# Performance work log

Hardware: AMD Instinct MI355X
Metric: run time of the kernel (lower is better)

The kernel has to match this reference:

```python
import jax, jax.numpy as jnp
import numpy as np

HEAD = 4      # args.head
N_HOPS = 2    # n_hops == gt_layer


def setup_inputs() -> dict:
    key = jax.random.key(0)
    ks = jax.random.split(key, 8)
    N, D, E, R = 100000, 64, 800000, 32
    entity_emb = jax.random.normal(ks[0], (N, D), dtype=jnp.float32) * 0.1
    weight = jax.random.normal(ks[1], (R - 1, D), dtype=jnp.float32) * 0.1
    Wq = jax.random.normal(ks[2], (N_HOPS, D, D), dtype=jnp.float32) * (1.0 / np.sqrt(D))
    Wk = jax.random.normal(ks[3], (N_HOPS, D, D), dtype=jnp.float32) * (1.0 / np.sqrt(D))
    Wv = jax.random.normal(ks[4], (N_HOPS, D, D), dtype=jnp.float32) * (1.0 / np.sqrt(D))
    edge_index = jax.random.randint(ks[5], (2, E), 0, N, dtype=jnp.int64 if jax.config.jax_enable_x64 else jnp.int32)
    edge_type = jax.random.randint(ks[6], (E,), 1, R, dtype=edge_index.dtype)  # in [1, R-1]
    return {"entity_emb": entity_emb, "weight": weight, "Wq": Wq, "Wk": Wk,
            "Wv": Wv, "edge_index": edge_index, "edge_type": edge_type}


def _kg_layer(rows, col_embeds, embeds, n_nodes, wq, wk, wv):
    # per-edge scaled-dot attention with index_add softmax normalization
    E, D = col_embeds.shape
    dh = D // HEAD
    q = (embeds[rows] @ wq).reshape(E, HEAD, dh)
    k = (col_embeds @ wk).reshape(E, HEAD, dh)
    v = (col_embeds @ wv).reshape(E, HEAD, dh)
    att = jnp.clip(jnp.einsum('ehd,ehd->eh', q, k), -10.0, 10.0)
    exp_att = jnp.exp(att)                                        # [E, H]
    att_norm = jax.ops.segment_sum(exp_att, rows, num_segments=n_nodes)[rows]
    a = exp_att / (att_norm + 1e-8)
    res = (a[..., None] * v).reshape(E, D)
    return jax.ops.segment_sum(res, rows, num_segments=n_nodes)   # [N, D]


def _scatter_softmax(x, index, n_seg):
    # numerically-stable softmax over edges grouped by index (torch_scatter.scatter_softmax)
    m = jax.ops.segment_max(x, index, num_segments=n_seg)
    e = jnp.exp(x - m[index])
    s = jax.ops.segment_sum(e, index, num_segments=n_seg)
    return e / (s[index] + 1e-16)


def reference(entity_emb, weight, Wq, Wk, Wv, edge_index, edge_type):
    N, D = entity_emb.shape
    head, tail = edge_index[0], edge_index[1]
    rel = weight[edge_type - 1]                                   # [E, D]
    emb = entity_emb
    res = entity_emb
    for layer in range(N_HOPS):
        neigh_rel = emb[tail] * rel                               # [E, D]
        kg_emb = _kg_layer(head, neigh_rel, emb, N, Wq[layer], Wk[layer], Wv[layer])
        # calculate_sim_hrt: product of L2 norms, squared (scalar per edge)
        hn = jnp.linalg.norm(kg_emb[head] * rel, axis=1)
        tn = jnp.linalg.norm(kg_emb[tail] * rel, axis=1)
        w = (hn * tn) ** 2                                        # [E]
        a = _scatter_softmax(w, head, N)                          # [E]
        neigh = a[:, None] * emb[tail]                            # [E, D]
        agg = jax.ops.segment_sum(neigh, head, num_segments=N)    # [N, D]
        # F.normalize + residual accumulation across hops
        emb = agg / jnp.maximum(jnp.linalg.norm(agg, axis=1, keepdims=True), 1e-12)
        res = res + emb
    return res
```

## Files before the change

### kernel.cpp

```cpp
#include <hip/hip_runtime.h>
#include <hip/hip_fp16.h>
#include <math.h>

#define BD 256
#define PBLK 2048

#define RED16(v) { v += __shfl_xor(v, 1, 64); v += __shfl_xor(v, 2, 64); \
                   v += __shfl_xor(v, 4, 64); v += __shfl_xor(v, 8, 64); }
#define REDQ(v)  { v += __shfl_xor(v, 16, 64); v += __shfl_xor(v, 32, 64); }

__device__ __forceinline__ __half2 shflxor_h2(__half2 v, int off) {
  int i = __shfl_xor(*(int*)&v, off, 64);
  return *(__half2*)&i;
}
#define REDQH(v)  { v = __hadd2(v, shflxor_h2(v, 16)); v = __hadd2(v, shflxor_h2(v, 32)); }
#define RED16H(v) { v = __hadd2(v, shflxor_h2(v, 1)); v = __hadd2(v, shflxor_h2(v, 2)); \
                    v = __hadd2(v, shflxor_h2(v, 4)); v = __hadd2(v, shflxor_h2(v, 8)); }

__global__ void k_init(const float4* __restrict__ ent, uint2* __restrict__ e16,
                       float4* __restrict__ out, int n4, int* __restrict__ deg, int N) {
  int i = blockIdx.x * BD + threadIdx.x;
  if (i < n4) {
    float4 v = ent[i];
    out[i] = v;
    __half2 h01 = __floats2half2_rn(v.x, v.y);
    __half2 h23 = __floats2half2_rn(v.z, v.w);
    uint2 st; st.x = *(unsigned int*)&h01; st.y = *(unsigned int*)&h23;
    e16[i] = st;
  }
  if (i < N) deg[i] = 0;
}

__global__ void k_deg(const int* __restrict__ head, int* __restrict__ deg, int E) {
  int e = blockIdx.x * BD + threadIdx.x;
  if (e < E) atomicAdd(&deg[head[e]], 1);
}

__global__ void k_scan_a(const int* __restrict__ deg, int* __restrict__ rowptr,
                         int* __restrict__ bsum, int N) {
  __shared__ int s[BD];
  int t = threadIdx.x, i = blockIdx.x * BD + t;
  int v = (i < N) ? deg[i] : 0;
  s[t] = v; __syncthreads();
  for (int off = 1; off < BD; off <<= 1) {
    int add = (t >= off) ? s[t - off] : 0;
    __syncthreads();
    s[t] += add;
    __syncthreads();
  }
  if (i < N) rowptr[i] = s[t] - v;
  if (t == BD - 1) bsum[blockIdx.x] = s[t];
}

__global__ void k_scan_b(const int* __restrict__ bsum, int* __restrict__ boff, int nb) {
  __shared__ int s[512];
  int t = threadIdx.x;
  int v = (t < nb) ? bsum[t] : 0;
  s[t] = v; __syncthreads();
  for (int off = 1; off < 512; off <<= 1) {
    int add = (t >= off) ? s[t - off] : 0;
    __syncthreads();
    s[t] += add;
    __syncthreads();
  }
  boff[t] = s[t] - v;
}

__global__ void k_scan_c(int* __restrict__ rowptr, int* __restrict__ cur,
                         const int* __restrict__ boff, int N, int E) {
  int i = blockIdx.x * BD + threadIdx.x;
  if (i < N) { int v = rowptr[i] + boff[blockIdx.x]; rowptr[i] = v; cur[i] = v; }
  if (i == 0) rowptr[N] = E;
}

__global__ void k_scatter(const int* __restrict__ head, const int* __restrict__ tail,
                          const int* __restrict__ etype,
                          int* __restrict__ cur, int2* __restrict__ epack, int E) {
  int e = blockIdx.x * BD + threadIdx.x;
  if (e < E) {
    int p = atomicAdd(&cur[head[e]], 1);
    epack[p] = make_int2(tail[e], etype[e] - 1);
  }
}

__global__ void k_m(const float* __restrict__ Wq, const float* __restrict__ Wk,
                    const float* __restrict__ weight,
                    float* __restrict__ Mf, __half* __restrict__ w16) {
  int tid = blockIdx.x * BD + threadIdx.x;
  int c = tid & 255;
  int m = tid >> 8;
  int i = c >> 2, h = c & 3;
  const float* wq = Wq + m * 64 + h * 16;
  const float* wk = Wk + i * 64 + h * 16;
  float acc = 0.f;
#pragma unroll
  for (int d = 0; d < 16; d++) acc = fmaf(wq[d], wk[d], acc);
  Mf[tid] = acc;
  if (tid < 2048) {
    int r = tid >> 6, j = tid & 63;
    w16[tid] = __float2half((r < 31) ? weight[r * 64 + j] : 0.f);
  }
}

__global__ __launch_bounds__(256) void k_g(const __half* __restrict__ e16,
                                           const float* __restrict__ Mf,
                                           uint2* __restrict__ Gh2, int N) {
  __shared__ float lM[64 * 256];
  int t = threadIdx.x;
  const float4* Mf4 = (const float4*)Mf;
  float4* lM4 = (float4*)lM;
  for (int i = t; i < 4096; i += BD) lM4[i] = Mf4[i];
  __syncthreads();
  int lane = t & 63, w = t >> 6;
  int nloc0 = blockIdx.x * 64 + w * 16;
#pragma unroll
  for (int b = 0; b < 2; b++) {
    int nl = nloc0 + b * 8;
    float4 acc[8];
#pragma unroll
    for (int ni = 0; ni < 8; ni++) acc[ni] = make_float4(0.f, 0.f, 0.f, 0.f);
#pragma unroll 4
    for (int m = 0; m < 64; m += 2) {
      float4 Mv0 = lM4[m * 64 + lane];
      float4 Mv1 = lM4[(m + 1) * 64 + lane];
#pragma unroll
      for (int ni = 0; ni < 8; ni++) {
        __half2 eh = *(const __half2*)(e16 + (size_t)(nl + ni) * 64 + m);
        float2 ef = __half22float2(eh);
        acc[ni].x = fmaf(ef.x, Mv0.x, acc[ni].x);
        acc[ni].y = fmaf(ef.x, Mv0.y, acc[ni].y);
        acc[ni].z = fmaf(ef.x, Mv0.z, acc[ni].z);
        acc[ni].w = fmaf(ef.x, Mv0.w, acc[ni].w);
        acc[ni].x = fmaf(ef.y, Mv1.x, acc[ni].x);
        acc[ni].y = fmaf(ef.y, Mv1.y, acc[ni].y);
        acc[ni].z = fmaf(ef.y, Mv1.z, acc[ni].z);
        acc[ni].w = fmaf(ef.y, Mv1.w, acc[ni].w);
      }
    }
#pragma unroll
    for (int ni = 0; ni < 8; ni++)
      if (nl + ni < N) {
        __half2 h01 = __floats2half2_rn(acc[ni].x, acc[ni].y);
        __half2 h23 = __floats2half2_rn(acc[ni].z, acc[ni].w);
        uint2 st;
        st.x = *(unsigned int*)&h01;
        st.y = *(unsigned int*)&h23;
        Gh2[(size_t)(nl + ni) * 64 + lane] = st;
      }
  }
}

__global__ __launch_bounds__(256) void k_fused(const uint2* __restrict__ e16,
                        const uint2* __restrict__ w16,
                        const uint4* __restrict__ Ghq, const float* __restrict__ Wv,
                        const int2* __restrict__ epack, const int* __restrict__ rowptr,
                        float* __restrict__ kg, int N) {
  __shared__ float SL[4 * 272];
  int t = threadIdx.x, lane = t & 63, w = t >> 6, q = lane >> 4, s = lane & 15;
  float* L = SL + w * 272;
  int wid = blockIdx.x * 4 + w, nw = gridDim.x * 4;
  const __half2 z2 = __float2half2_rn(0.f);
  for (int n = wid; n < N; n += nw) {
    uint4 ga = Ghq[(size_t)n * 32 + s * 2];
    uint4 gb = Ghq[(size_t)n * 32 + s * 2 + 1];
    __half2 c0h01 = *(__half2*)&ga.x, c0h23 = *(__half2*)&ga.y;
    __half2 c1h01 = *(__half2*)&ga.z, c1h23 = *(__half2*)&ga.w;
    __half2 c2h01 = *(__half2*)&gb.x, c2h23 = *(__half2*)&gb.y;
    __half2 c3h01 = *(__half2*)&gb.z, c3h23 = *(__half2*)&gb.w;

    int base = rowptr[n], deg = rowptr[n + 1] - base;
    float4 den = make_float4(0.f, 0.f, 0.f, 0.f);
    __half2 S0a = z2, S0b = z2, S1a = z2, S1b = z2;
    __half2 S2a = z2, S2b = z2, S3a = z2, S3b = z2;
    for (int g0 = 0; g0 < deg; g0 += 4) {
      int k = g0 + q;
      bool valid = (k < deg);
      int kk = min(k, deg - 1);
      int2 p = epack[base + kk];
      uint2 eu = e16[(size_t)p.x * 16 + s];
      uint2 ru = w16[(size_t)p.y * 16 + s];
      __half2 x01 = __hmul2(*(__half2*)&eu.x, *(__half2*)&ru.x);
      __half2 x23 = __hmul2(*(__half2*)&eu.y, *(__half2*)&ru.y);
      __half2 b0 = __low2half2(x01), b1 = __high2half2(x01);
      __half2 b2 = __low2half2(x23), b3 = __high2half2(x23);
      __half2 a01 = __hmul2(b0, c0h01);
      a01 = __hfma2(b1, c1h01, a01);
      a01 = __hfma2(b2, c2h01, a01);
      a01 = __hfma2(b3, c3h01, a01);
      __half2 a23 = __hmul2(b0, c0h23);
      a23 = __hfma2(b1, c1h23, a23);
      a23 = __hfma2(b2, c2h23, a23);
      a23 = __hfma2(b3, c3h23, a23);
      RED16H(a01) RED16H(a23)
      float2 fa01 = __half22float2(a01);
      float2 fa23 = __half22float2(a23);
      fa01.x = fminf(10.f, fmaxf(-10.f, fa01.x));
      fa01.y = fminf(10.f, fmaxf(-10.f, fa01.y));
      fa23.x = fminf(10.f, fmaxf(-10.f, fa23.x));
      fa23.y = fminf(10.f, fmaxf(-10.f, fa23.y));
      float4 ev;
      ev.x = valid ? __expf(fa01.x) : 0.f;
      ev.y = valid ? __expf(fa01.y) : 0.f;
      ev.z = valid ? __expf(fa23.x) : 0.f;
      ev.w = valid ? __expf(fa23.y) : 0.f;
      den.x += ev.x; den.y += ev.y; den.z += ev.z; den.w += ev.w;
      __half2 e01 = __floats2half2_rn(ev.x, ev.y);
      __half2 e23 = __floats2half2_rn(ev.z, ev.w);
      S0a = __hfma2(e01, b0, S0a); S0b = __hfma2(e23, b0, S0b);
      S1a = __hfma2(e01, b1, S1a); S1b = __hfma2(e23, b1, S1b);
      S2a = __hfma2(e01, b2, S2a); S2b = __hfma2(e23, b2, S2b);
      S3a = __hfma2(e01, b3, S3a); S3b = __hfma2(e23, b3, S3b);
    }
    REDQ(den.x) REDQ(den.y) REDQ(den.z) REDQ(den.w)
    REDQH(S0a) REDQH(S0b) REDQH(S1a) REDQH(S1b)
    REDQH(S2a) REDQH(S2b) REDQH(S3a) REDQH(S3b)
    float4 inv;
    inv.x = 1.f / (den.x + 1e-8f); inv.y = 1.f / (den.y + 1e-8f);
    inv.z = 1.f / (den.z + 1e-8f); inv.w = 1.f / (den.w + 1e-8f);
    float2 c0, c1;
    c0 = __half22float2(S0a); c1 = __half22float2(S0b);
    float s0h0 = c0.x * inv.x, s0h1 = c0.y * inv.y, s0h2 = c1.x * inv.z, s0h3 = c1.y * inv.w;
    c0 = __half22float2(S1a); c1 = __half22float2(S1b);
    float s1h0 = c0.x * inv.x, s1h1 = c0.y * inv.y, s1h2 = c1.x * inv.z, s1h3 = c1.y * inv.w;
    c0 = __half22float2(S2a); c1 = __half22float2(S2b);
    float s2h0 = c0.x * inv.x, s2h1 = c0.y * inv.y, s2h2 = c1.x * inv.z, s2h3 = c1.y * inv.w;
    c0 = __half22float2(S3a); c1 = __half22float2(S3b);
    float s3h0 = c0.x * inv.x, s3h1 = c0.y * inv.y, s3h2 = c1.x * inv.z, s3h3 = c1.y * inv.w;
    if (q == 0) {
      *(float4*)(L +       s * 4) = make_float4(s0h0, s1h0, s2h0, s3h0);
      *(float4*)(L +  68 + s * 4) = make_float4(s0h1, s1h1, s2h1, s3h1);
      *(float4*)(L + 136 + s * 4) = make_float4(s0h2, s1h2, s2h2, s3h2);
      *(float4*)(L + 204 + s * 4) = make_float4(s0h3, s1h3, s2h3, s3h3);
    }
    const float4* L4 = (const float4*)(L + q * 68);
    float acc = 0.f;
#pragma unroll
    for (int i4 = 0; i4 < 16; i4++) {
      float4 Lv = L4[i4];
      acc = fmaf(Lv.x, Wv[(i4 * 4 + 0) * 64 + lane], acc);
      acc = fmaf(Lv.y, Wv[(i4 * 4 + 1) * 64 + lane], acc);
      acc = fmaf(Lv.z, Wv[(i4 * 4 + 2) * 64 + lane], acc);
      acc = fmaf(Lv.w, Wv[(i4 * 4 + 3) * 64 + lane], acc);
    }
    kg[(size_t)n * 64 + lane] = acc;
  }
}

__global__ __launch_bounds__(256) void k_d(const float4* __restrict__ kg4,
                    const float* __restrict__ weight,
                    float* __restrict__ D, int N) {
  __shared__ float R2T[64 * 32];
  __shared__ float KG2[64 * 68];
  int t = threadIdx.x;
  for (int i = t; i < 2048; i += BD) {
    int j = i >> 5, r = i & 31;
    float v = (r < 31) ? weight[r * 64 + j] : 0.f;
    R2T[i] = v * v;
  }
  int nbase = blockIdx.x * 64;
  const float4* src = kg4 + (size_t)nbase * 16;
#pragma unroll
  for (int i = 0; i < 4; i++) {
    int idx = t + i * 256;
    float4 v = src[idx];
    float* dst = KG2 + (idx >> 4) * 68 + (idx & 15) * 4;
    dst[0] = v.x * v.x; dst[1] = v.y * v.y; dst[2] = v.z * v.z; dst[3] = v.w * v.w;
  }
  __syncthreads();
  int r = t & 31, ng = t >> 5;
  float acc[8] = {0.f, 0.f, 0.f, 0.f, 0.f, 0.f, 0.f, 0.f};
  const float* kbase = KG2 + ng * 8 * 68;
#pragma unroll 4
  for (int j4 = 0; j4 < 16; j4++) {
    float r0 = R2T[(j4 * 4 + 0) * 32 + r];
    float r1 = R2T[(j4 * 4 + 1) * 32 + r];
    float r2 = R2T[(j4 * 4 + 2) * 32 + r];
    float r3 = R2T[(j4 * 4 + 3) * 32 + r];
#pragma unroll
    for (int ni = 0; ni < 8; ni++) {
      float4 kv = *(const float4*)(kbase + ni * 68 + j4 * 4);
      acc[ni] = fmaf(kv.w, r3, fmaf(kv.z, r2, fmaf(kv.y, r1, fmaf(kv.x, r0, acc[ni]))));
    }
  }
  if (r < 31) {
    int nlim = N - nbase;
#pragma unroll
    for (int ni = 0; ni < 8; ni++) {
      int nl = ng * 8 + ni;
      if (nl < nlim) D[(size_t)(nbase + nl) * 32 + r] = acc[ni];
    }
  }
}

__global__ __launch_bounds__(256) void k_aggnorm(const uint2* __restrict__ e16,
                          const float* __restrict__ D,
                          const int2* __restrict__ epack, const int* __restrict__ rowptr,
                          uint2* __restrict__ en16, float* __restrict__ out, int N) {
  __shared__ float DnL[4 * 32];
  int t = threadIdx.x, lane = t & 63, w = t >> 6, q = lane >> 4, s = lane & 15;
  float* Dn = DnL + w * 32;
  int wid = blockIdx.x * 4 + w, nw = gridDim.x * 4;
  for (int n = wid; n < N; n += nw) {
    int base = rowptr[n], deg = rowptr[n + 1] - base;
    if (lane < 32) Dn[lane] = (lane < 31) ? D[(size_t)n * 32 + lane] : 0.f;
    float4 agg = make_float4(0.f, 0.f, 0.f, 0.f);
    float sacc = 0.f;
    for (int g0 = 0; g0 < deg; g0 += 4) {
      int k = g0 + q;
      bool valid = (k < deg);
      int kk = min(k, deg - 1);
      int2 p = epack[base + kk];
      uint2 eu = e16[(size_t)p.x * 16 + s];
      float wv = Dn[p.y] * D[(size_t)p.x * 32 + p.y];
      float2 ef0 = __half22float2(*(__half2*)&eu.x);
      float2 ef1 = __half22float2(*(__half2*)&eu.y);
      float a = valid ? __expf(wv) : 0.f;
      sacc += a;
      agg.x = fmaf(a, ef0.x, agg.x);
      agg.y = fmaf(a, ef0.y, agg.y);
      agg.z = fmaf(a, ef1.x, agg.z);
      agg.w = fmaf(a, ef1.y, agg.w);
    }
    REDQ(sacc)
    REDQ(agg.x) REDQ(agg.y) REDQ(agg.z) REDQ(agg.w)
    float sinv = 1.f / (sacc + 1e-16f);
    agg.x *= sinv; agg.y *= sinv; agg.z *= sinv; agg.w *= sinv;
    float ss = agg.x * agg.x + agg.y * agg.y + agg.z * agg.z + agg.w * agg.w;
    RED16(ss)
    float nr = fmaxf(sqrtf(ss), 1e-12f);
    float rin = 1.f / nr;
    float4 en;
    en.x = agg.x * rin; en.y = agg.y * rin; en.z = agg.z * rin; en.w = agg.w * rin;
    if (q == 0) {
      __half2 h01 = __floats2half2_rn(en.x, en.y);
      __half2 h23 = __floats2half2_rn(en.z, en.w);
      uint2 st; st.x = *(unsigned int*)&h01; st.y = *(unsigned int*)&h23;
      en16[(size_t)n * 16 + s] = st;
      float4* oo = (float4*)(out + (size_t)n * 64) + s;
      float4 ov = *oo;
      ov.x += en.x; ov.y += en.y; ov.z += en.z; ov.w += en.w;
      *oo = ov;
    }
  }
}

extern "C" void kernel_launch(void* const* d_in, const int* in_sizes, int n_in,
                              void* d_out, int out_size, void* d_ws, size_t ws_size,
                              hipStream_t stream) {
  const float* ent    = (const float*)d_in[0];
  const float* weight = (const float*)d_in[1];
  const float* Wq     = (const float*)d_in[2];
  const float* Wk     = (const float*)d_in[3];
  const float* Wv     = (const float*)d_in[4];
  const int*   eidx   = (const int*)d_in[5];
  const int*   etype  = (const int*)d_in[6];
  int N = in_sizes[0] / 64;
  int E = in_sizes[6];
  const int* head = eidx;
  const int* tail = eidx + E;

  float* ws    = (float*)d_ws;
  size_t o = 0;
  float* e16A  = ws + o; o += (size_t)N * 32;
  float* e16B  = ws + o; o += (size_t)N * 32;
  float* kgbuf = ws + o; o += (size_t)N * 64;
  float* Gbuf  = ws + o; o += (size_t)N * 128;
  float* Mf    = ws + o; o += 64 * 256;
  float* w16   = ws + o; o += 1024;
  int2* epack  = (int2*)(ws + o); o += (size_t)E * 2;
  int* rowptr  = (int*)(ws + o); o += N + 1;
  int* deg     = (int*)(ws + o); o += N;
  int* cur     = (int*)(ws + o); o += N;
  int* bsum    = (int*)(ws + o); o += 512;
  int* boff    = (int*)(ws + o); o += 512;
  float* Dbuf  = Gbuf;

  int n4  = N * 64 / 4;
  int bl4 = (n4 + BD - 1) / BD;
  int ebl = (E + BD - 1) / BD;
  int sbl = (N + BD - 1) / BD;

  k_init<<<bl4, BD, 0, stream>>>((const float4*)ent, (uint2*)e16A, (float4*)d_out,
                                 n4, deg, N);
  k_deg    <<<ebl, BD, 0, stream>>>(head, deg, E);
  k_scan_a <<<sbl, BD, 0, stream>>>(deg, rowptr, bsum, N);
  k_scan_b <<<1, 512, 0, stream>>>(bsum, boff, sbl);
  k_scan_c <<<sbl, BD, 0, stream>>>(rowptr, cur, boff, N, E);
  k_scatter<<<ebl, BD, 0, stream>>>(head, tail, etype, cur, epack, E);

  float* emb = e16A;
  float* alt = e16B;
  for (int l = 0; l < 2; l++) {
    const float* wq = Wq + (size_t)l * 64 * 64;
    const float* wk = Wk + (size_t)l * 64 * 64;
    const float* wv = Wv + (size_t)l * 64 * 64;

    k_m<<<64, BD, 0, stream>>>(wq, wk, weight, Mf, (__half*)w16);
    k_g<<<(N + 63) / 64, BD, 0, stream>>>((const __half*)emb, Mf, (uint2*)Gbuf, N);
    k_fused<<<PBLK, BD, 0, stream>>>((const uint2*)emb, (const uint2*)w16,
                                     (const uint4*)Gbuf, wv, epack, rowptr, kgbuf, N);
    k_d<<<(N + 63) / 64, BD, 0, stream>>>((const float4*)kgbuf, weight, Dbuf, N);
    k_aggnorm<<<PBLK, BD, 0, stream>>>((const uint2*)emb, Dbuf, epack, rowptr,
                                       (uint2*)alt, (float*)d_out, N);
    float* tmp = emb; emb = alt; alt = tmp;
  }
}
```

Baseline: 612.4 us.

## Pack edge tail and type into one int; precompute aggnorm edge weights per lane

```diff
diff --git a/kernel.cpp b/kernel.cpp
--- a/kernel.cpp
+++ b/kernel.cpp
@@ -3,6 +3,7 @@
 #include <math.h>
 
 #define BD 256
+#define CAP 192
 #define PBLK 2048
 
 #define RED16(v) { v += __shfl_xor(v, 1, 64); v += __shfl_xor(v, 2, 64); \
@@ -75,11 +76,11 @@
 
 __global__ void k_scatter(const int* __restrict__ head, const int* __restrict__ tail,
                           const int* __restrict__ etype,
-                          int* __restrict__ cur, int2* __restrict__ epack, int E) {
+                          int* __restrict__ cur, int* __restrict__ epk, int E) {
   int e = blockIdx.x * BD + threadIdx.x;
   if (e < E) {
     int p = atomicAdd(&cur[head[e]], 1);
-    epack[p] = make_int2(tail[e], etype[e] - 1);
+    epk[p] = tail[e] * 32 + (etype[e] - 1);
   }
 }
 
@@ -153,7 +154,7 @@
 __global__ __launch_bounds__(256) void k_fused(const uint2* __restrict__ e16,
                         const uint2* __restrict__ w16,
                         const uint4* __restrict__ Ghq, const float* __restrict__ Wv,
-                        const int2* __restrict__ epack, const int* __restrict__ rowptr,
+                        const int* __restrict__ epk, const int* __restrict__ rowptr,
                         float* __restrict__ kg, int N) {
   __shared__ float SL[4 * 272];
   int t = threadIdx.x, lane = t & 63, w = t >> 6, q = lane >> 4, s = lane & 15;
@@ -176,9 +177,9 @@
       int k = g0 + q;
       bool valid = (k < deg);
       int kk = min(k, deg - 1);
-      int2 p = epack[base + kk];
-      uint2 eu = e16[(size_t)p.x * 16 + s];
-      uint2 ru = w16[(size_t)p.y * 16 + s];
+      int cmb = epk[base + kk];
+      uint2 eu = e16[(size_t)(cmb >> 5) * 16 + s];
+      uint2 ru = w16[((cmb & 31) << 4) + s];
       __half2 x01 = __hmul2(*(__half2*)&eu.x, *(__half2*)&ru.x);
       __half2 x23 = __hmul2(*(__half2*)&eu.y, *(__half2*)&ru.y);
       __half2 b0 = __low2half2(x01), b1 = __high2half2(x01);
@@ -294,10 +295,12 @@
 
 __global__ __launch_bounds__(256) void k_aggnorm(const uint2* __restrict__ e16,
                           const float* __restrict__ D,
-                          const int2* __restrict__ epack, const int* __restrict__ rowptr,
+                          const int* __restrict__ epk, const int* __restrict__ rowptr,
                           uint2* __restrict__ en16, float* __restrict__ out, int N) {
+  __shared__ float wls[4 * CAP];
   __shared__ float DnL[4 * 32];
   int t = threadIdx.x, lane = t & 63, w = t >> 6, q = lane >> 4, s = lane & 15;
+  float* wl = wls + w * CAP;
   float* Dn = DnL + w * 32;
   int wid = blockIdx.x * 4 + w, nw = gridDim.x * 4;
   for (int n = wid; n < N; n += nw) {
@@ -305,23 +308,28 @@
     if (lane < 32) Dn[lane] = (lane < 31) ? D[(size_t)n * 32 + lane] : 0.f;
     float4 agg = make_float4(0.f, 0.f, 0.f, 0.f);
     float sacc = 0.f;
+    for (int k = lane; k < deg; k += 64) {
+      int cmb = epk[base + k];
+      float a = __expf(Dn[cmb & 31] * D[cmb]);
+      if (k < CAP) wl[k] = a;
+      sacc += a;
+    }
+    RED16(sacc) REDQ(sacc)
     for (int g0 = 0; g0 < deg; g0 += 4) {
       int k = g0 + q;
       bool valid = (k < deg);
       int kk = min(k, deg - 1);
-      int2 p = epack[base + kk];
-      uint2 eu = e16[(size_t)p.x * 16 + s];
-      float wv = Dn[p.y] * D[(size_t)p.x * 32 + p.y];
+      int cmb = epk[base + kk];
+      float a = valid ? ((kk < CAP) ? wl[kk]
+                                    : __expf(Dn[cmb & 31] * D[cmb])) : 0.f;
+      uint2 eu = e16[(size_t)(cmb >> 5) * 16 + s];
       float2 ef0 = __half22float2(*(__half2*)&eu.x);
       float2 ef1 = __half22float2(*(__half2*)&eu.y);
-      float a = valid ? __expf(wv) : 0.f;
-      sacc += a;
       agg.x = fmaf(a, ef0.x, agg.x);
       agg.y = fmaf(a, ef0.y, agg.y);
       agg.z = fmaf(a, ef1.x, agg.z);
       agg.w = fmaf(a, ef1.y, agg.w);
     }
-    REDQ(sacc)
     REDQ(agg.x) REDQ(agg.y) REDQ(agg.z) REDQ(agg.w)
     float sinv = 1.f / (sacc + 1e-16f);
     agg.x *= sinv; agg.y *= sinv; agg.z *= sinv; agg.w *= sinv;
@@ -367,7 +375,7 @@
   float* Gbuf  = ws + o; o += (size_t)N * 128;
   float* Mf    = ws + o; o += 64 * 256;
   float* w16   = ws + o; o += 1024;
-  int2* epack  = (int2*)(ws + o); o += (size_t)E * 2;
+  int* epk     = (int*)(ws + o); o += (size_t)E;
   int* rowptr  = (int*)(ws + o); o += N + 1;
   int* deg     = (int*)(ws + o); o += N;
   int* cur     = (int*)(ws + o); o += N;
@@ -386,7 +394,7 @@
   k_scan_a <<<sbl, BD, 0, stream>>>(deg, rowptr, bsum, N);
   k_scan_b <<<1, 512, 0, stream>>>(bsum, boff, sbl);
   k_scan_c <<<sbl, BD, 0, stream>>>(rowptr, cur, boff, N, E);
-  k_scatter<<<ebl, BD, 0, stream>>>(head, tail, etype, cur, epack, E);
+  k_scatter<<<ebl, BD, 0, stream>>>(head, tail, etype, cur, epk, E);
 
   float* emb = e16A;
   float* alt = e16B;
@@ -398,9 +406,9 @@
     k_m<<<64, BD, 0, stream>>>(wq, wk, weight, Mf, (__half*)w16);
     k_g<<<(N + 63) / 64, BD, 0, stream>>>((const __half*)emb, Mf, (uint2*)Gbuf, N);
     k_fused<<<PBLK, BD, 0, stream>>>((const uint2*)emb, (const uint2*)w16,
-                                     (const uint4*)Gbuf, wv, epack, rowptr, kgbuf, N);
+                                     (const uint4*)Gbuf, wv, epk, rowptr, kgbuf, N);
     k_d<<<(N + 63) / 64, BD, 0, stream>>>((const float4*)kgbuf, weight, Dbuf, N);
-    k_aggnorm<<<PBLK, BD, 0, stream>>>((const uint2*)emb, Dbuf, epack, rowptr,
+    k_aggnorm<<<PBLK, BD, 0, stream>>>((const uint2*)emb, Dbuf, epk, rowptr,
                                        (uint2*)alt, (float*)d_out, N);
     float* tmp = emb; emb = alt; alt = tmp;
   }
```

Result: faster. 577.4 us (-5.7%).
